# Kernel optimization log

Hardware: AMD Instinct MI355X
Metric: run time of the kernel (lower is better)

The kernel has to match this reference:

```python
import jax, jax.numpy as jnp
import numpy as np

V, H, S, U, UC, E = 30000, 128, 32, 128, 10000, 300000
LAMBDA_T, LAMBDA_S = 0.1, 100.0
DAY = 86400.0


def setup_inputs() -> dict:
    key = jax.random.key(0)
    k = jax.random.split(key, 20)
    sc = 0.02
    x = jax.random.randint(k[0], (S, U), 0, V)
    # timestamps: cumulative positive intervals so t[i] >= t[j] for j <= i
    t = jnp.cumsum(jax.random.uniform(k[1], (S, U), minval=60.0, maxval=3600.0), axis=0)
    t_slot = jax.random.randint(k[2], (S, U), 0, 168)
    s = jax.random.normal(k[3], (S, U, 2)) * 0.1
    y_t = t + 600.0
    y_t_slot = jax.random.randint(k[4], (S, U), 0, 168)
    y_s = jax.random.normal(k[5], (S, U, 2)) * 0.1
    h = jnp.zeros((U, H), jnp.float32)
    active_user = jax.random.randint(k[6], (U,), 0, UC)
    graph_rows = jax.random.randint(k[7], (E,), 0, V)
    graph_cols = jax.random.randint(k[8], (E,), 0, V)
    enc_emb = jax.random.normal(k[9], (V, H)) * sc
    user_emb = jax.random.normal(k[10], (UC, H)) * sc
    pref_emb = jax.random.normal(k[11], (1, 2 * H)) * sc
    proj_W = jax.random.normal(k[12], (H, 2 * H)) * sc
    proj_b = jnp.zeros((2 * H,), jnp.float32)
    W_ih = jax.random.normal(k[13], (H, H)) * sc
    W_hh = jax.random.normal(k[14], (H, H)) * sc
    b_rnn = jnp.zeros((H,), jnp.float32)
    fc_W = jax.random.normal(k[15], (2 * H, V)) * sc
    fc_b = jnp.zeros((V,), jnp.float32)
    return dict(x=x, t=t, t_slot=t_slot, s=s, y_t=y_t, y_t_slot=y_t_slot, y_s=y_s,
                h=h, active_user=active_user, graph_rows=graph_rows, graph_cols=graph_cols,
                enc_emb=enc_emb, user_emb=user_emb, pref_emb=pref_emb,
                proj_W=proj_W, proj_b=proj_b, W_ih=W_ih, W_hh=W_hh, b_rnn=b_rnn,
                fc_W=fc_W, fc_b=fc_b)


def reference(x, t, t_slot, s, y_t, y_t_slot, y_s, h, active_user, graph_rows, graph_cols,
              enc_emb, user_emb, pref_emb, proj_W, proj_b, W_ih, W_hh, b_rnn, fc_W, fc_b):
    # --- random-walk-normalized graph conv: D^{-1}(A + I) @ enc_emb ---
    ones_e = jnp.ones(graph_rows.shape, enc_emb.dtype)
    deg = jax.ops.segment_sum(ones_e, graph_rows, num_segments=V) + 1.0  # +1 self loop
    agg = jax.ops.segment_sum(enc_emb[graph_cols], graph_rows, num_segments=V)
    encoder_weight = (agg + enc_emb) / deg[:, None]  # [V, H]

    x_emb = encoder_weight[x]  # [S, U, H]

    # --- vanilla tanh RNN over the sequence dim ---
    def step(hprev, xt):
        hn = jnp.tanh(xt @ W_ih.T + hprev @ W_hh.T + b_rnn)
        return hn, hn
    h_last, out = jax.lax.scan(step, h, x_emb)  # out: [S, U, H]

    # --- user preference similarity (TransE-style: user + pref vs loc) ---
    p_u = user_emb[active_user]                       # [U, H]
    p_proj = jnp.tanh(p_u @ proj_W + proj_b)          # [U, 2H]
    x_proj = jnp.tanh(x_emb @ proj_W + proj_b)        # [S, U, 2H]
    sim = jax.nn.sigmoid(jnp.einsum('ud,sud->us', p_proj + pref_emb[0], x_proj))  # [U, S]

    # --- causal spatio-temporal decay weighted average (the O(S^2) loop, vectorized) ---
    dist_t = t[:, None, :] - t[None, :, :]                       # [S, S, U] (i, j, u)
    dist_s = jnp.linalg.norm(s[:, None] - s[None, :], axis=-1)   # [S, S, U]
    a = 0.5 * (jnp.cos(dist_t * (2.0 * jnp.pi / DAY)) + 1.0) * jnp.exp(-(dist_t / DAY) * LAMBDA_T)
    b = jnp.exp(-dist_s * LAMBDA_S)
    w = (a * b + 1e-10) * jnp.transpose(sim)[None, :, :]         # scale by sim[u, j]
    causal = jnp.tril(jnp.ones((S, S), w.dtype))
    w = w * causal[:, :, None]
    sum_w = jnp.sum(w, axis=1)                                   # [S, U]
    out_w = jnp.einsum('iju,juh->iuh', w, out) / sum_w[..., None]  # [S, U, H]

    # --- concat user embedding, final projection to location logits ---
    out_pu = jnp.concatenate([out_w, jnp.broadcast_to(p_u, (S, U, H))], axis=-1)  # [S, U, 2H]
    y_linear = out_pu @ fc_W + fc_b  # [S, U, V]
    return y_linear, h_last
```

## Files before the change

### kernel.cpp

```cpp
#include <hip/hip_runtime.h>
#include <hip/hip_bf16.h>

#define VV 30000
#define HH 128
#define SS 32
#define UU 128
#define EE 300000

typedef unsigned short u16;
typedef unsigned int u32;

__device__ __forceinline__ u16 f2b(float f){ union{float f; u32 i;} v; v.f=f; u32 x=v.i; x += 0x7fffu + ((x>>16)&1u); return (u16)(x>>16); }

typedef __bf16 bf16x8 __attribute__((ext_vector_type(8)));
typedef float f32x4 __attribute__((ext_vector_type(4)));

__device__ __forceinline__ void gl_lds16(const void* g, void* l){
  __builtin_amdgcn_global_load_lds((const __attribute__((address_space(1))) u32*)g,
                                   (__attribute__((address_space(3))) u32*)l, 16, 0, 0);
}

__global__ __launch_bounds__(256) void k_flag(const int* __restrict__ x, int* __restrict__ needed){
  int i = blockIdx.x*256 + threadIdx.x;
  needed[x[i]] = 1;
}

__global__ __launch_bounds__(256) void k_deg(const int* __restrict__ rows, int* __restrict__ deg){
  int e = blockIdx.x*256 + threadIdx.x;
  if (e < EE) atomicAdd(&deg[rows[e]], 1);
}

__global__ __launch_bounds__(256) void k_agg(const int* __restrict__ rows, const int* __restrict__ cols,
    const float* __restrict__ enc, const int* __restrict__ needed, float* __restrict__ agg){
  int e = blockIdx.x*2 + (threadIdx.x >> 7);
  int hh = threadIdx.x & 127;
  int r = rows[e];
  if (!needed[r]) return;
  int c = cols[e];
  atomicAdd(&agg[(size_t)r*HH + hh], enc[(size_t)c*HH + hh]);
}

__global__ __launch_bounds__(128) void k_xemb(const int* __restrict__ x, const float* __restrict__ agg,
    const float* __restrict__ enc, const int* __restrict__ deg, float* __restrict__ xemb){
  int su = blockIdx.x, hh = threadIdx.x;
  int v = x[su];
  float d = (float)(deg[v] + 1);
  xemb[su*HH + hh] = (agg[(size_t)v*HH + hh] + enc[(size_t)v*HH + hh]) / d;
}

__global__ __launch_bounds__(256) void k_rnn(const float* __restrict__ xemb,
     const float* __restrict__ h0, const float* __restrict__ Wih, const float* __restrict__ Whh,
     const float* __restrict__ brnn, float* __restrict__ outws, float* __restrict__ hlast)
{
  int u = blockIdx.x, t = threadIdx.x;
  int d = t & 127, half = t >> 7;
  __shared__ float xbuf[128], hbuf[128], part[256];
  float wf[128];
  const float4* wr4 = (const float4*)((half ? Whh : Wih) + d*HH);
  #pragma unroll
  for(int i=0;i<32;i++){
    float4 q = wr4[i];
    wf[4*i+0]=q.x; wf[4*i+1]=q.y; wf[4*i+2]=q.z; wf[4*i+3]=q.w;
  }
  float bias = 0.f;
  if (t < 128){ hbuf[t] = h0[u*HH + t]; bias = brnn[t]; }
  for(int s0=0; s0<SS; ++s0){
    if (t < 128) xbuf[t] = xemb[(s0*UU + u)*HH + t];
    __syncthreads();
    const float4* vp = (const float4*)(half ? hbuf : xbuf);
    float acc = 0.f;
    #pragma unroll
    for(int k4=0;k4<32;k4++){
      float4 vv = vp[k4];
      acc += wf[4*k4+0]*vv.x + wf[4*k4+1]*vv.y + wf[4*k4+2]*vv.z + wf[4*k4+3]*vv.w;
    }
    part[t] = acc;
    __syncthreads();
    if (t < 128){
      float hn = tanhf(part[t] + part[t+128] + bias);
      outws[(s0*UU + u)*HH + t] = hn;
      hbuf[t] = hn;
      if (s0 == SS-1) hlast[u*HH + t] = hn;
    }
    __syncthreads();
  }
}

__global__ __launch_bounds__(256) void k_pproj(const int* __restrict__ au, const float* __restrict__ uemb,
    const float* __restrict__ projW, const float* __restrict__ projb, const float* __restrict__ pref,
    float* __restrict__ sp)
{
  int u = blockIdx.x, d = threadIdx.x;
  __shared__ float pl[128];
  int a = au[u];
  if (d < 128) pl[d] = uemb[(size_t)a*HH + d];
  __syncthreads();
  float acc = 0.f;
  #pragma unroll 4
  for(int k=0;k<128;k++) acc += pl[k]*projW[k*256 + d];
  sp[u*256 + d] = tanhf(acc + projb[d]) + pref[d];
}

__global__ __launch_bounds__(256) void k_xprojsim(const float* __restrict__ xemb,
   const float* __restrict__ projW, const float* __restrict__ projb,
   const float* __restrict__ sp, float* __restrict__ sim)
{
  int su = blockIdx.x; int s0 = su >> 7, u = su & 127;
  int d = threadIdx.x;
  __shared__ float xl[128];
  __shared__ float red[4];
  if (d < 128) xl[d] = xemb[su*HH + d];
  __syncthreads();
  float acc = 0.f;
  #pragma unroll 4
  for(int k=0;k<128;k++) acc += xl[k]*projW[k*256 + d];
  float xp = tanhf(acc + projb[d]);
  float val = xp * sp[u*256 + d];
  for(int off=32; off>0; off>>=1) val += __shfl_down(val, off, 64);
  if ((d & 63) == 0) red[d>>6] = val;
  __syncthreads();
  if (d == 0){
    float sum = red[0]+red[1]+red[2]+red[3];
    sim[u*SS + s0] = 1.f/(1.f + expf(-sum));
  }
}

__global__ __launch_bounds__(256) void k_decay(const float* __restrict__ t_in, const float* __restrict__ s_in,
    const float* __restrict__ sim, const float* __restrict__ outws,
    const float* __restrict__ uemb, const int* __restrict__ au, u16* __restrict__ outpu)
{
  int u = blockIdx.x, tid = threadIdx.x;
  __shared__ float outL[SS*HH];
  __shared__ float wm[SS*SS];
  __shared__ float tl[SS], sx[SS], sy[SS], sml[SS], swv[SS];
  __shared__ u16 pub[HH];
  for(int idx=tid; idx<SS*HH; idx+=256){
    int j = idx >> 7, hh = idx & 127;
    outL[idx] = outws[(j*UU + u)*HH + hh];
  }
  if (tid < SS){
    tl[tid]  = t_in[tid*UU + u];
    sx[tid]  = s_in[(tid*UU + u)*2 + 0];
    sy[tid]  = s_in[(tid*UU + u)*2 + 1];
    sml[tid] = sim[u*SS + tid];
  }
  if (tid < HH) pub[tid] = f2b(uemb[(size_t)au[u]*HH + tid]);
  __syncthreads();
  for(int p=tid; p<SS*SS; p+=256){
    int i = p >> 5, j = p & 31;
    float wv = 0.f;
    if (j <= i){
      float dt = tl[i] - tl[j];
      float a = 0.5f*(cosf(dt * 7.2722052166430399e-05f) + 1.0f) * expf(dt * -1.1574074074074074e-06f);
      float dx = sx[i]-sx[j], dy = sy[i]-sy[j];
      float b = expf(-100.0f * sqrtf(dx*dx + dy*dy));
      wv = (a*b + 1e-10f) * sml[j];
    }
    wm[p] = wv;
  }
  __syncthreads();
  if (tid < SS){
    float ssum = 0.f;
    for(int j=0;j<=tid;j++) ssum += wm[tid*32 + j];
    swv[tid] = ssum;
  }
  __syncthreads();
  for(int p=tid; p<SS*HH; p+=256){
    int i = p >> 7, hh = p & 127;
    float accv = 0.f;
    for(int j=0;j<=i;j++) accv += wm[i*32 + j]*outL[j*128 + hh];
    size_t row = (size_t)(i*UU + u)*256;
    outpu[row + hh] = f2b(accv / swv[i]);
    outpu[row + 128 + hh] = pub[hh];
  }
}

__global__ __launch_bounds__(256) void k_transp(const float* __restrict__ fcW, u16* __restrict__ fcwT){
  __shared__ u16 tl[64*65];
  int n0 = blockIdx.x*64, k0 = blockIdx.y*64;
  int tid = threadIdx.x;
  {
    int nn = tid & 63, k4 = tid >> 6;
    for (int r = 0; r < 16; ++r) {
      int kk = r*4 + k4;
      int n = n0 + nn;
      u16 v = 0;
      if (n < VV) v = f2b(fcW[(size_t)(k0+kk)*VV + n]);
      tl[kk*65 + nn] = v;
    }
  }
  __syncthreads();
  {
    int kk = tid & 63, n4 = tid >> 6;
    for (int r = 0; r < 16; ++r) {
      int nn = r*4 + n4;
      fcwT[(size_t)(n0+nn)*256 + k0 + kk] = tl[kk*65 + nn];
    }
  }
}

__global__ __launch_bounds__(256) void k_gemm(const u16* __restrict__ A, const u16* __restrict__ BT,
    const float* __restrict__ bias, float* __restrict__ C)
{
  __shared__ __align__(16) char smem[34816];
  char* As = smem;
  char* Bs = smem + 8192;
  const int tid = threadIdx.x;
  const int lane = tid & 63;
  const int w = tid >> 6;
  const int n0 = blockIdx.x * 128;
  const int m0 = blockIdx.y * 128;
  const int wr = w >> 1, wc = w & 1;

  f32x4 acc[16];
  #pragma unroll
  for(int i=0;i<16;i++) acc[i] = (f32x4){0.f,0.f,0.f,0.f};

  const char* Ab = (const char*)A;
  const char* Bb = (const char*)BT;
  const int c0 = w*2, c1 = c0+1;
  const int r0 = c0*16 + (lane>>2), r1 = c1*16 + (lane>>2);
  const int bco = (lane&3)*16;

  for(int kt=0; kt<8; ++kt){
    __syncthreads();
    gl_lds16(Ab + (size_t)(m0+r0)*512 + kt*64 + bco, As + c0*1024);
    gl_lds16(Ab + (size_t)(m0+r1)*512 + kt*64 + bco, As + c1*1024);
    gl_lds16(Bb + (size_t)(n0+r0)*512 + kt*64 + bco, Bs + c0*1024);
    gl_lds16(Bb + (size_t)(n0+r1)*512 + kt*64 + bco, Bs + c1*1024);
    __syncthreads();
    bf16x8 af[4], bg[4];
    const int kb = (lane>>4)*16;
    const int fr = lane & 15;
    #pragma unroll
    for(int mt=0;mt<4;++mt) af[mt] = *(const bf16x8*)(As + (wr*64 + mt*16 + fr)*64 + kb);
    #pragma unroll
    for(int nt=0;nt<4;++nt) bg[nt] = *(const bf16x8*)(Bs + (wc*64 + nt*16 + fr)*64 + kb);
    #pragma unroll
    for(int mt=0;mt<4;++mt)
      #pragma unroll
      for(int nt=0;nt<4;++nt)
        acc[mt*4+nt] = __builtin_amdgcn_mfma_f32_16x16x32_bf16(af[mt], bg[nt], acc[mt*4+nt], 0, 0, 0);
  }

  const int fr = lane & 15;
  float bl[4];
  #pragma unroll
  for(int nt=0;nt<4;++nt){
    int n = n0 + wc*64 + nt*16 + fr;
    bl[nt] = bias[n < VV ? n : 0];
  }
  float* Csf = (float*)smem;
  #pragma unroll
  for(int pass=0; pass<2; ++pass){
    __syncthreads();
    if (wr == pass){
      #pragma unroll
      for(int mt=0;mt<4;++mt){
        #pragma unroll
        for(int nt=0;nt<4;++nt){
          int col = wc*64 + nt*16 + fr;
          #pragma unroll
          for(int r=0;r<4;++r){
            int lrow = mt*16 + (lane>>4)*4 + r;
            Csf[lrow*136 + col] = acc[mt*4+nt][r] + bl[nt];
          }
        }
      }
    }
    __syncthreads();
    int lrow = tid >> 2, q = tid & 3;
    int grow = m0 + pass*64 + lrow;
    const float4* src = (const float4*)(Csf + lrow*136 + q*32);
    float* dst = C + (size_t)grow*VV + n0 + q*32;
    #pragma unroll
    for(int j=0;j<8;++j){
      int n = n0 + q*32 + j*4;
      if (n < VV) *(float4*)(dst + j*4) = src[j];
    }
  }
}

extern "C" void kernel_launch(void* const* d_in, const int* in_sizes, int n_in,
                              void* d_out, int out_size, void* d_ws, size_t ws_size,
                              hipStream_t stream)
{
  (void)in_sizes; (void)n_in; (void)out_size; (void)ws_size;
  const int*   x      = (const int*)d_in[0];
  const float* t_in   = (const float*)d_in[1];
  const float* s_in   = (const float*)d_in[3];
  const float* h0     = (const float*)d_in[7];
  const int*   au     = (const int*)d_in[8];
  const int*   grows  = (const int*)d_in[9];
  const int*   gcols  = (const int*)d_in[10];
  const float* enc    = (const float*)d_in[11];
  const float* uemb   = (const float*)d_in[12];
  const float* pref   = (const float*)d_in[13];
  const float* projW  = (const float*)d_in[14];
  const float* projb  = (const float*)d_in[15];
  const float* Wih    = (const float*)d_in[16];
  const float* Whh    = (const float*)d_in[17];
  const float* brnn   = (const float*)d_in[18];
  const float* fcW    = (const float*)d_in[19];
  const float* fcb    = (const float*)d_in[20];
  float* yf = (float*)d_out;
  float* hlast = yf + (size_t)SS*UU*VV;
  char* ws = (char*)d_ws;
  int*   needed = (int*)(ws + 0);
  int*   deg    = (int*)(ws + 120000);
  float* agg    = (float*)(ws + 240000);
  u16*   fcwT   = (u16*)(ws + 0);
  float* xemb   = (float*)(ws + 15600000);
  float* outws  = (float*)(ws + 17697152);
  float* sp     = (float*)(ws + 19794304);
  float* sim    = (float*)(ws + 19925376);
  u16*   outpu  = (u16*)(ws + 19941760);

  hipMemsetAsync(ws, 0, 15600000, stream);
  hipLaunchKernelGGL(k_flag,     dim3(16),      dim3(256), 0, stream, x, needed);
  hipLaunchKernelGGL(k_deg,      dim3((EE+255)/256), dim3(256), 0, stream, grows, deg);
  hipLaunchKernelGGL(k_agg,      dim3(EE/2),    dim3(256), 0, stream, grows, gcols, enc, needed, agg);
  hipLaunchKernelGGL(k_xemb,     dim3(SS*UU),   dim3(128), 0, stream, x, agg, enc, deg, xemb);
  hipLaunchKernelGGL(k_transp,   dim3(470,4),   dim3(256), 0, stream, fcW, fcwT);
  hipLaunchKernelGGL(k_rnn,      dim3(UU),      dim3(256), 0, stream, xemb, h0, Wih, Whh, brnn, outws, hlast);
  hipLaunchKernelGGL(k_pproj,    dim3(UU),      dim3(256), 0, stream, au, uemb, projW, projb, pref, sp);
  hipLaunchKernelGGL(k_xprojsim, dim3(SS*UU),   dim3(256), 0, stream, xemb, projW, projb, sp, sim);
  hipLaunchKernelGGL(k_decay,    dim3(UU),      dim3(256), 0, stream, t_in, s_in, sim, outws, uemb, au, outpu);
  hipLaunchKernelGGL(k_gemm,     dim3(235,32),  dim3(256), 0, stream, outpu, fcwT, fcb, yf);
}
```

Measured before the change: 879.0 us.

## Restructure GEMM with larger swizzled LDS tiles and direct nontemporal stores; fuse graph prep kernels

The output GEMM now loads 128x256 K-slices into XOR-swizzled LDS in two steps instead of eight 64-wide steps, which cuts barriers. It also writes results straight from registers with nontemporal stores instead of staging through LDS. The grid is swapped so M varies fastest, letting neighbouring blocks share B tiles. Separately, the flag and degree kernels are fused, the edge aggregation uses a grid-stride loop, and the RNN and projection dot products use multiple accumulators. The tradeoffs are higher LDS use (64KB) that may lower occupancy, and uncoalesced scalar stores to the 491MB output.

```diff
diff --git a/kernel.cpp b/kernel.cpp
--- a/kernel.cpp
+++ b/kernel.cpp
@@ -20,24 +20,24 @@
                                    (__attribute__((address_space(3))) u32*)l, 16, 0, 0);
 }
 
-__global__ __launch_bounds__(256) void k_flag(const int* __restrict__ x, int* __restrict__ needed){
-  int i = blockIdx.x*256 + threadIdx.x;
-  needed[x[i]] = 1;
-}
-
-__global__ __launch_bounds__(256) void k_deg(const int* __restrict__ rows, int* __restrict__ deg){
-  int e = blockIdx.x*256 + threadIdx.x;
-  if (e < EE) atomicAdd(&deg[rows[e]], 1);
+__global__ __launch_bounds__(256) void k_flagdeg(const int* __restrict__ x, const int* __restrict__ rows,
+    int* __restrict__ needed, int* __restrict__ deg){
+  int gid = blockIdx.x*256 + threadIdx.x;
+  if (gid < SS*UU) needed[x[gid]] = 1;
+  if (gid < EE) atomicAdd(&deg[rows[gid]], 1);
 }
 
 __global__ __launch_bounds__(256) void k_agg(const int* __restrict__ rows, const int* __restrict__ cols,
     const float* __restrict__ enc, const int* __restrict__ needed, float* __restrict__ agg){
-  int e = blockIdx.x*2 + (threadIdx.x >> 7);
-  int hh = threadIdx.x & 127;
-  int r = rows[e];
-  if (!needed[r]) return;
-  int c = cols[e];
-  atomicAdd(&agg[(size_t)r*HH + hh], enc[(size_t)c*HH + hh]);
+  int hh  = threadIdx.x & 127;
+  int sub = threadIdx.x >> 7;
+  int stride = gridDim.x * 2;
+  for (int e = blockIdx.x*2 + sub; e < EE; e += stride){
+    int r = rows[e];
+    if (!needed[r]) continue;
+    int c = cols[e];
+    atomicAdd(&agg[(size_t)r*HH + hh], enc[(size_t)c*HH + hh]);
+  }
 }
 
 __global__ __launch_bounds__(128) void k_xemb(const int* __restrict__ x, const float* __restrict__ agg,
@@ -68,13 +68,16 @@
     if (t < 128) xbuf[t] = xemb[(s0*UU + u)*HH + t];
     __syncthreads();
     const float4* vp = (const float4*)(half ? hbuf : xbuf);
-    float acc = 0.f;
-    #pragma unroll
-    for(int k4=0;k4<32;k4++){
-      float4 vv = vp[k4];
-      acc += wf[4*k4+0]*vv.x + wf[4*k4+1]*vv.y + wf[4*k4+2]*vv.z + wf[4*k4+3]*vv.w;
-    }
-    part[t] = acc;
+    float a0=0.f, a1=0.f, a2=0.f, a3=0.f;
+    #pragma unroll
+    for(int k4=0;k4<32;k4+=4){
+      float4 v0 = vp[k4+0], v1 = vp[k4+1], v2 = vp[k4+2], v3 = vp[k4+3];
+      a0 += wf[4*k4+0]*v0.x + wf[4*k4+1]*v0.y + wf[4*k4+2]*v0.z + wf[4*k4+3]*v0.w;
+      a1 += wf[4*k4+4]*v1.x + wf[4*k4+5]*v1.y + wf[4*k4+6]*v1.z + wf[4*k4+7]*v1.w;
+      a2 += wf[4*k4+8]*v2.x + wf[4*k4+9]*v2.y + wf[4*k4+10]*v2.z + wf[4*k4+11]*v2.w;
+      a3 += wf[4*k4+12]*v3.x + wf[4*k4+13]*v3.y + wf[4*k4+14]*v3.z + wf[4*k4+15]*v3.w;
+    }
+    part[t] = (a0+a1)+(a2+a3);
     __syncthreads();
     if (t < 128){
       float hn = tanhf(part[t] + part[t+128] + bias);
@@ -111,10 +114,13 @@
   __shared__ float red[4];
   if (d < 128) xl[d] = xemb[su*HH + d];
   __syncthreads();
-  float acc = 0.f;
+  float a0 = 0.f, a1 = 0.f;
   #pragma unroll 4
-  for(int k=0;k<128;k++) acc += xl[k]*projW[k*256 + d];
-  float xp = tanhf(acc + projb[d]);
+  for(int k=0;k<128;k+=2){
+    a0 += xl[k]*projW[k*256 + d];
+    a1 += xl[k+1]*projW[(k+1)*256 + d];
+  }
+  float xp = tanhf(a0 + a1 + projb[d]);
   float val = xp * sp[u*256 + d];
   for(int off=32; off>0; off>>=1) val += __shfl_down(val, off, 64);
   if ((d & 63) == 0) red[d>>6] = val;
@@ -202,15 +208,14 @@
 __global__ __launch_bounds__(256) void k_gemm(const u16* __restrict__ A, const u16* __restrict__ BT,
     const float* __restrict__ bias, float* __restrict__ C)
 {
-  __shared__ __align__(16) char smem[34816];
-  char* As = smem;
-  char* Bs = smem + 8192;
-  const int tid = threadIdx.x;
+  __shared__ __align__(16) char As[32768];
+  __shared__ __align__(16) char Bs[32768];
+  const int tid  = threadIdx.x;
   const int lane = tid & 63;
-  const int w = tid >> 6;
-  const int n0 = blockIdx.x * 128;
-  const int m0 = blockIdx.y * 128;
-  const int wr = w >> 1, wc = w & 1;
+  const int wv   = tid >> 6;
+  const int wr = wv >> 1, wc = wv & 1;
+  const int m0 = blockIdx.x * 128;
+  const int n0 = blockIdx.y * 128;
 
   f32x4 acc[16];
   #pragma unroll
@@ -218,65 +223,64 @@
 
   const char* Ab = (const char*)A;
   const char* Bb = (const char*)BT;
-  const int c0 = w*2, c1 = c0+1;
-  const int r0 = c0*16 + (lane>>2), r1 = c1*16 + (lane>>2);
-  const int bco = (lane&3)*16;
-
-  for(int kt=0; kt<8; ++kt){
-    __syncthreads();
-    gl_lds16(Ab + (size_t)(m0+r0)*512 + kt*64 + bco, As + c0*1024);
-    gl_lds16(Ab + (size_t)(m0+r1)*512 + kt*64 + bco, As + c1*1024);
-    gl_lds16(Bb + (size_t)(n0+r0)*512 + kt*64 + bco, Bs + c0*1024);
-    gl_lds16(Bb + (size_t)(n0+r1)*512 + kt*64 + bco, Bs + c1*1024);
-    __syncthreads();
-    bf16x8 af[4], bg[4];
-    const int kb = (lane>>4)*16;
-    const int fr = lane & 15;
-    #pragma unroll
-    for(int mt=0;mt<4;++mt) af[mt] = *(const bf16x8*)(As + (wr*64 + mt*16 + fr)*64 + kb);
-    #pragma unroll
-    for(int nt=0;nt<4;++nt) bg[nt] = *(const bf16x8*)(Bs + (wc*64 + nt*16 + fr)*64 + kb);
-    #pragma unroll
-    for(int mt=0;mt<4;++mt)
+  const int srow = tid >> 4;
+  const int scol = ((tid & 15) ^ srow) << 4;
+
+  const int fr = lane & 15;
+  const int kq = lane >> 4;
+
+  for (int kt = 0; kt < 2; ++kt){
+    __syncthreads();
+    #pragma unroll
+    for (int i = 0; i < 8; ++i)
+      gl_lds16(Ab + (size_t)(m0 + i*16 + srow)*512 + kt*256 + scol, As + i*4096 + wv*1024);
+    #pragma unroll
+    for (int i = 0; i < 8; ++i)
+      gl_lds16(Bb + (size_t)(n0 + i*16 + srow)*512 + kt*256 + scol, Bs + i*4096 + wv*1024);
+    __syncthreads();
+
+    #pragma unroll
+    for (int ks = 0; ks < 4; ++ks){
+      bf16x8 af[4], bg[4];
+      const int p = ((ks*4 + kq) ^ fr) << 4;
       #pragma unroll
-      for(int nt=0;nt<4;++nt)
-        acc[mt*4+nt] = __builtin_amdgcn_mfma_f32_16x16x32_bf16(af[mt], bg[nt], acc[mt*4+nt], 0, 0, 0);
-  }
-
-  const int fr = lane & 15;
+      for (int mt = 0; mt < 4; ++mt)
+        af[mt] = *(const bf16x8*)(As + (wr*64 + mt*16 + fr)*256 + p);
+      #pragma unroll
+      for (int nt = 0; nt < 4; ++nt)
+        bg[nt] = *(const bf16x8*)(Bs + (wc*64 + nt*16 + fr)*256 + p);
+      #pragma unroll
+      for (int mt = 0; mt < 4; ++mt)
+        #pragma unroll
+        for (int nt = 0; nt < 4; ++nt)
+          acc[mt*4+nt] = __builtin_amdgcn_mfma_f32_16x16x32_bf16(af[mt], bg[nt], acc[mt*4+nt], 0, 0, 0);
+    }
+  }
+
+  const int n_base = n0 + wc*64;
   float bl[4];
   #pragma unroll
   for(int nt=0;nt<4;++nt){
-    int n = n0 + wc*64 + nt*16 + fr;
-    bl[nt] = bias[n < VV ? n : 0];
-  }
-  float* Csf = (float*)smem;
+    int n = n_base + nt*16 + fr;
+    bl[nt] = (n < VV) ? bias[n] : 0.f;
+  }
+  const bool full = (n0 + 128 <= VV);
   #pragma unroll
-  for(int pass=0; pass<2; ++pass){
-    __syncthreads();
-    if (wr == pass){
-      #pragma unroll
-      for(int mt=0;mt<4;++mt){
+  for(int mt=0;mt<4;++mt){
+    #pragma unroll
+    for(int r=0;r<4;++r){
+      size_t rowoff = (size_t)(m0 + wr*64 + mt*16 + kq*4 + r) * VV;
+      if (full){
+        #pragma unroll
+        for(int nt=0;nt<4;++nt)
+          __builtin_nontemporal_store(acc[mt*4+nt][r] + bl[nt], &C[rowoff + n_base + nt*16 + fr]);
+      } else {
         #pragma unroll
         for(int nt=0;nt<4;++nt){
-          int col = wc*64 + nt*16 + fr;
-          #pragma unroll
-          for(int r=0;r<4;++r){
-            int lrow = mt*16 + (lane>>4)*4 + r;
-            Csf[lrow*136 + col] = acc[mt*4+nt][r] + bl[nt];
-          }
+          int n = n_base + nt*16 + fr;
+          if (n < VV) __builtin_nontemporal_store(acc[mt*4+nt][r] + bl[nt], &C[rowoff + n]);
         }
       }
-    }
-    __syncthreads();
-    int lrow = tid >> 2, q = tid & 3;
-    int grow = m0 + pass*64 + lrow;
-    const float4* src = (const float4*)(Csf + lrow*136 + q*32);
-    float* dst = C + (size_t)grow*VV + n0 + q*32;
-    #pragma unroll
-    for(int j=0;j<8;++j){
-      int n = n0 + q*32 + j*4;
-      if (n < VV) *(float4*)(dst + j*4) = src[j];
     }
   }
 }
@@ -317,14 +321,13 @@
   u16*   outpu  = (u16*)(ws + 19941760);
 
   hipMemsetAsync(ws, 0, 15600000, stream);
-  hipLaunchKernelGGL(k_flag,     dim3(16),      dim3(256), 0, stream, x, needed);
-  hipLaunchKernelGGL(k_deg,      dim3((EE+255)/256), dim3(256), 0, stream, grows, deg);
-  hipLaunchKernelGGL(k_agg,      dim3(EE/2),    dim3(256), 0, stream, grows, gcols, enc, needed, agg);
+  hipLaunchKernelGGL(k_flagdeg,  dim3(1172),    dim3(256), 0, stream, x, grows, needed, deg);
+  hipLaunchKernelGGL(k_agg,      dim3(2048),    dim3(256), 0, stream, grows, gcols, enc, needed, agg);
   hipLaunchKernelGGL(k_xemb,     dim3(SS*UU),   dim3(128), 0, stream, x, agg, enc, deg, xemb);
   hipLaunchKernelGGL(k_transp,   dim3(470,4),   dim3(256), 0, stream, fcW, fcwT);
   hipLaunchKernelGGL(k_rnn,      dim3(UU),      dim3(256), 0, stream, xemb, h0, Wih, Whh, brnn, outws, hlast);
   hipLaunchKernelGGL(k_pproj,    dim3(UU),      dim3(256), 0, stream, au, uemb, projW, projb, pref, sp);
   hipLaunchKernelGGL(k_xprojsim, dim3(SS*UU),   dim3(256), 0, stream, xemb, projW, projb, sp, sim);
   hipLaunchKernelGGL(k_decay,    dim3(UU),      dim3(256), 0, stream, t_in, s_in, sim, outws, uemb, au, outpu);
-  hipLaunchKernelGGL(k_gemm,     dim3(235,32),  dim3(256), 0, stream, outpu, fcwT, fcb, yf);
-}
+  hipLaunchKernelGGL(k_gemm,     dim3(32,235),  dim3(256), 0, stream, outpu, fcwT, fcb, yf);
+}
```

Result: faster. 774.9 us (-11.8%).
